# Kernel tuning notes

Hardware: AMD Instinct MI355X
Metric: run time of the kernel (lower is better)

The kernel has to match this reference:

```python
import jax, jax.numpy as jnp
import numpy as np

C_S, C_Z, S = 384, 128, 1024
D = 32
H = C_S // D
INF = 1e9
EPS = 1e-5


def rmsnorm(x, w, eps=EPS):
    ms = jnp.mean(jnp.square(x), axis=-1, keepdims=True)
    return x * jax.lax.rsqrt(ms + eps) * w


def setup_inputs() -> dict:
    key = jax.random.key(0)
    ks = jax.random.split(key, 12)
    inv_s = 1.0 / np.sqrt(C_S)
    inv_z = 1.0 / np.sqrt(C_Z)
    return {
        "s": jax.random.normal(ks[0], (S, C_S), jnp.float32),
        "z": jax.random.normal(ks[1], (S, S, C_Z), jnp.float32),
        "z_mask": jax.random.randint(ks[2], (S, S), 0, 2, jnp.int32),
        "w_s": jnp.ones((C_S,), jnp.float32),
        "w_z": jnp.ones((C_Z,), jnp.float32),
        "Wz": jax.random.normal(ks[3], (C_Z, H), jnp.float32) * inv_z,
        "Wq": jax.random.normal(ks[4], (C_S, H * D), jnp.float32) * inv_s,
        "Wk": jax.random.normal(ks[5], (C_S, H * D), jnp.float32) * inv_s,
        "Wv": jax.random.normal(ks[6], (C_S, H * D), jnp.float32) * inv_s,
        "Wg": jax.random.normal(ks[7], (C_S, C_S), jnp.float32) * inv_s,
        "bg": jnp.zeros((C_S,), jnp.float32),
        "Wo": jax.random.normal(ks[8], (C_S, C_S), jnp.float32) * inv_s,
        "bo": jnp.zeros((C_S,), jnp.float32),
    }


def reference(s, z, z_mask, w_s, w_z, Wz, Wq, Wk, Wv, Wg, bg, Wo, bo):
    s_n = rmsnorm(s, w_s)                      # [S, c_s]
    z_n = rmsnorm(z, w_z)                      # [S, S, c_z]
    q = (s_n @ Wq).reshape(S, H, D).transpose(1, 0, 2)  # [H, S, D]
    k = (s_n @ Wk).reshape(S, H, D).transpose(1, 0, 2)
    v = (s_n @ Wv).reshape(S, H, D).transpose(1, 0, 2)
    g = s_n @ Wg + bg                          # [S, c_s] (no sigmoid in source)
    # pair bias [H, S, S] + additive mask
    bias = jnp.einsum('ijc,ch->hij', z_n, Wz)
    bias = bias + jnp.where(z_mask != 0, 0.0, -INF)[None]
    scores = jnp.einsum('hid,hjd->hij', q, k) * (1.0 / np.sqrt(D)) + bias
    attn = jax.nn.softmax(scores, axis=-1)
    out = jnp.einsum('hij,hjd->hid', attn, v)  # [H, S, D]
    o = out.transpose(1, 0, 2).reshape(S, H * D)
    return ((o @ Wo + bo) * g).astype(jnp.float32)
```

## Files before the change

kernel.cpp:

```cpp
#include <hip/hip_runtime.h>
#include <hip/hip_fp16.h>

#define SQ 1024

typedef __attribute__((ext_vector_type(8))) short short8;
typedef __attribute__((ext_vector_type(4))) float f32x4;
typedef __attribute__((ext_vector_type(4))) int i32x4;
typedef __attribute__((ext_vector_type(2))) unsigned int u32x2;

#define MFMA16(a,b,c) __builtin_amdgcn_mfma_f32_16x16x32_bf16((a),(b),(c),0,0,0)

static __device__ __forceinline__ float bf2f(unsigned short u){
  union { unsigned int i; float f; } v; v.i = ((unsigned int)u) << 16; return v.f;
}
static __device__ __forceinline__ unsigned short f2bf(float f){
  union { float fv; unsigned int i; } v; v.fv = f;
  unsigned int r = v.i + 0x7fffu + ((v.i >> 16) & 1u);
  return (unsigned short)(r >> 16);
}
static __device__ __forceinline__ void split_store(float val, unsigned short* hi, unsigned short* lo, int idx){
  unsigned short h = f2bf(val);
  hi[idx] = h;
  lo[idx] = f2bf(val - bf2f(h));
}

static __device__ __forceinline__ void pack8(f32x4 u0, f32x4 u0b, short8& AHv, short8& ALv){
  unsigned int x0 = __float_as_uint(u0.x),  x1 = __float_as_uint(u0.y);
  unsigned int x2 = __float_as_uint(u0.z),  x3 = __float_as_uint(u0.w);
  unsigned int y0 = __float_as_uint(u0b.x), y1 = __float_as_uint(u0b.y);
  unsigned int y2 = __float_as_uint(u0b.z), y3 = __float_as_uint(u0b.w);
  float r0 = u0.x  - __uint_as_float(x0 & 0xffff0000u);
  float r1 = u0.y  - __uint_as_float(x1 & 0xffff0000u);
  float r2 = u0.z  - __uint_as_float(x2 & 0xffff0000u);
  float r3 = u0.w  - __uint_as_float(x3 & 0xffff0000u);
  float s0 = u0b.x - __uint_as_float(y0 & 0xffff0000u);
  float s1 = u0b.y - __uint_as_float(y1 & 0xffff0000u);
  float s2 = u0b.z - __uint_as_float(y2 & 0xffff0000u);
  float s3 = u0b.w - __uint_as_float(y3 & 0xffff0000u);
  union { unsigned int d[4]; short8 v; } AH, AL;
  AH.d[0] = (x0 >> 16) | (x1 & 0xffff0000u);
  AH.d[1] = (x2 >> 16) | (x3 & 0xffff0000u);
  AH.d[2] = (y0 >> 16) | (y1 & 0xffff0000u);
  AH.d[3] = (y2 >> 16) | (y3 & 0xffff0000u);
  AL.d[0] = (__float_as_uint(r0) >> 16) | (__float_as_uint(r1) & 0xffff0000u);
  AL.d[1] = (__float_as_uint(r2) >> 16) | (__float_as_uint(r3) & 0xffff0000u);
  AL.d[2] = (__float_as_uint(s0) >> 16) | (__float_as_uint(s1) & 0xffff0000u);
  AL.d[3] = (__float_as_uint(s2) >> 16) | (__float_as_uint(s3) & 0xffff0000u);
  AHv = AH.v; ALv = AL.v;
}

#define COMP4(v,e) ((e)==0?(v).x:(e)==1?(v).y:(e)==2?(v).z:(v).w)

#define QK_SCALE 0.17677669529663687f
#define MASK_NEG -60000.0f

__global__ __launch_bounds__(256) void prep_all(
    const float* __restrict__ Wq, const float* __restrict__ Wk,
    const float* __restrict__ Wv, const float* __restrict__ Wg,
    const float* __restrict__ Wo,
    const float* __restrict__ wz, const float* __restrict__ Wz,
    const float* __restrict__ s, const float* __restrict__ w_s,
    unsigned short* __restrict__ wt_hi, unsigned short* __restrict__ wt_lo,
    unsigned short* __restrict__ wwh, unsigned short* __restrict__ wwl2,
    unsigned short* __restrict__ s_hi, unsigned short* __restrict__ s_lo){
  __shared__ __align__(16) float tile[32][33];
  int bid = blockIdx.x;
  int t = threadIdx.x;
  if (bid < 720){
    int bx = bid % 60, by = bid / 60;
    int tx = t & 31, ty = t >> 5;
    int nt = bx * 32, kt = by * 32;
    int nb = nt / 384;
    const float* W = (nb==0)?Wq:(nb==1)?Wk:(nb==2)?Wv:(nb==3)?Wg:Wo;
    int nn0 = nt - nb*384;
    #pragma unroll
    for (int yy=0; yy<4; yy++){
      int k = kt + ty + yy*8;
      tile[ty + yy*8][tx] = W[k*384 + nn0 + tx];
    }
    __syncthreads();
    #pragma unroll
    for (int yy=0; yy<4; yy++){
      int n = nt + ty + yy*8;
      int k = kt + tx;
      float v = tile[tx][ty + yy*8];
      split_store(v, wt_hi, wt_lo, n*384 + k);
    }
  } else if (bid == 720){
    for (int idx = t; idx < 2048; idx += 256){
      int c = idx >> 4, h = idx & 15;
      float val = (h < 12) ? wz[c]*Wz[c*12 + h] : 0.f;
      unsigned short hh = f2bf(val);
      wwh[idx] = hh;
      wwl2[idx] = f2bf(val - bf2f(hh));
    }
  } else {
    int wv = t >> 6, lane = t & 63;
    int row = (bid - 721)*4 + wv;
    const float* sr = s + row*384;
    float v[6]; float ss = 0.f;
    #pragma unroll
    for (int q=0;q<6;q++){ v[q] = sr[lane + q*64]; ss += v[q]*v[q]; }
    #pragma unroll
    for (int m=1;m<64;m<<=1) ss += __shfl_xor(ss, m);
    float rs = rsqrtf(ss*(1.f/384.f) + 1e-5f);
    #pragma unroll
    for (int q=0;q<6;q++){
      int c = lane + q*64;
      split_store(v[q]*rs*w_s[c], s_hi, s_lo, row*384 + c);
    }
  }
}

__global__ __launch_bounds__(256,3) void qkvg_bias_k(
    const unsigned short* __restrict__ Ah, const unsigned short* __restrict__ Al,
    const unsigned short* __restrict__ Bh2, const unsigned short* __restrict__ Bl2,
    const float* __restrict__ bg,
    unsigned short* __restrict__ q_hi, unsigned short* __restrict__ q_lo,
    unsigned short* __restrict__ k_hi, unsigned short* __restrict__ k_lo,
    unsigned short* __restrict__ v_hi, unsigned short* __restrict__ v_lo,
    float* __restrict__ g,
    const float* __restrict__ z, const int* __restrict__ zm,
    const unsigned short* __restrict__ wwh, const unsigned short* __restrict__ wwl2,
    __half* __restrict__ biasH){
  __shared__ __align__(16) unsigned short lah[64*40], lal[64*40], lbh[64*40], lbl[64*40];
  __shared__ __align__(16) float rsbuf[4*16];
  int bid = blockIdx.x;
  int t = threadIdx.x, w = t >> 6, lane = t & 63;
  int fr = lane & 15, fg = lane >> 4;

  if (bid < 384){
    int m0 = (bid / 24) * 64, n0 = (bid % 24) * 64;
    f32x4 z4 = {0.f,0.f,0.f,0.f};
    f32x4 acc[4] = {z4, z4, z4, z4};
    int sr = t >> 2, sc = (t & 3) << 3;
    for (int k0 = 0; k0 < 384; k0 += 32){
      *(short8*)&lah[sr*40 + sc] = *(const short8*)&Ah[(m0+sr)*384 + k0 + sc];
      *(short8*)&lal[sr*40 + sc] = *(const short8*)&Al[(m0+sr)*384 + k0 + sc];
      *(short8*)&lbh[sr*40 + sc] = *(const short8*)&Bh2[(n0+sr)*384 + k0 + sc];
      *(short8*)&lbl[sr*40 + sc] = *(const short8*)&Bl2[(n0+sr)*384 + k0 + sc];
      __syncthreads();
      short8 a_h = *(short8*)&lah[(w*16+fr)*40 + (fg<<3)];
      short8 a_l = *(short8*)&lal[(w*16+fr)*40 + (fg<<3)];
      #pragma unroll
      for (int cf=0; cf<4; cf++){
        short8 b_h = *(short8*)&lbh[(cf*16+fr)*40 + (fg<<3)];
        short8 b_l = *(short8*)&lbl[(cf*16+fr)*40 + (fg<<3)];
        acc[cf] = MFMA16(a_h, b_h, acc[cf]);
        acc[cf] = MFMA16(a_h, b_l, acc[cf]);
        acc[cf] = MFMA16(a_l, b_h, acc[cf]);
      }
      __syncthreads();
    }
    int sec = n0 / 384;
    int nb0 = n0 - sec*384;
    #pragma unroll
    for (int cf=0; cf<4; cf++){
      #pragma unroll
      for (int jj=0; jj<4; jj++){
        int row = m0 + w*16 + (fg<<2) + jj;
        int nn = nb0 + cf*16 + fr;
        float val = acc[cf][jj];
        int hh = nn >> 5, dd = nn & 31;
        if (sec == 0)      split_store(val*QK_SCALE, q_hi, q_lo, (hh<<15) + (row<<5) + dd);
        else if (sec == 1) split_store(val, k_hi, k_lo, (hh<<15) + (row<<5) + dd);
        else if (sec == 2) split_store(val, v_hi, v_lo, (hh<<15) + dd*SQ + row);
        else               g[row*384 + nn] = val + bg[nn];
      }
    }
    return;
  }

  int wid = ((bid - 384) << 2) + w;

  short8 Bh[4], Bl[4];
  #pragma unroll
  for (int kt=0; kt<4; kt++){
    #pragma unroll
    for (int e=0; e<8; e++){
      int c = kt*32 + (fg<<3) + e;
      Bh[kt][e] = (short)wwh[(c<<4) + fr];
      Bl[kt][e] = (short)wwl2[(c<<4) + fr];
    }
  }

  f32x4 cA[8], cB[8];
  i32x4 zmA, zmB;

  #define LOADS(DST, ZMD, ST)                                             \
    {                                                                     \
      size_t tile = (size_t)(ST)*8192 + (size_t)wid;                      \
      const float* p = z + tile*2048 + fr*128 + (fg<<3);                  \
      DST[0] = __builtin_nontemporal_load((const f32x4*)(p));             \
      DST[1] = __builtin_nontemporal_load((const f32x4*)(p+4));           \
      DST[2] = __builtin_nontemporal_load((const f32x4*)(p+32));          \
      DST[3] = __builtin_nontemporal_load((const f32x4*)(p+36));          \
      DST[4] = __builtin_nontemporal_load((const f32x4*)(p+64));          \
      DST[5] = __builtin_nontemporal_load((const f32x4*)(p+68));          \
      DST[6] = __builtin_nontemporal_load((const f32x4*)(p+96));          \
      DST[7] = __builtin_nontemporal_load((const f32x4*)(p+100));         \
      int ii = (int)(tile >> 6), jj0 = ((int)tile & 63) << 4;             \
      ZMD = *(const i32x4*)&zm[ii*SQ + jj0 + (fg<<2)];                    \
    }

  #define COMPUTE(SRC, ZMD, ST)                                              \
    {                                                                        \
      f32x4 acc0 = {0.f,0.f,0.f,0.f};                                        \
      float ssq0 = 0.f;                                                      \
      _Pragma("unroll")                                                      \
      for (int kt=0; kt<4; kt++){                                            \
        f32x4 u0  = SRC[kt*2];                                               \
        f32x4 u0b = SRC[kt*2+1];                                             \
        ssq0 = fmaf(u0.x,u0.x,ssq0);   ssq0 = fmaf(u0.y,u0.y,ssq0);          \
        ssq0 = fmaf(u0.z,u0.z,ssq0);   ssq0 = fmaf(u0.w,u0.w,ssq0);          \
        ssq0 = fmaf(u0b.x,u0b.x,ssq0); ssq0 = fmaf(u0b.y,u0b.y,ssq0);        \
        ssq0 = fmaf(u0b.z,u0b.z,ssq0); ssq0 = fmaf(u0b.w,u0b.w,ssq0);        \
        short8 AHv, ALv;                                                     \
        pack8(u0, u0b, AHv, ALv);                                            \
        acc0 = MFMA16(AHv, Bh[kt], acc0);                                    \
        acc0 = MFMA16(AHv, Bl[kt], acc0);                                    \
        acc0 = MFMA16(ALv, Bh[kt], acc0);                                    \
      }                                                                      \
      ssq0 += __shfl_xor(ssq0, 16); ssq0 += __shfl_xor(ssq0, 32);            \
      if (lane < 16)                                                         \
        rsbuf[w*16 + lane] = rsqrtf(ssq0*(1.0f/128.0f) + 1e-5f);             \
      int jo = fg << 2;                                                      \
      f32x4 rs0 = *(const f32x4*)&rsbuf[w*16 + jo];                          \
      f32x4 mk0;                                                             \
      mk0.x = (ZMD.x != 0) ? 0.f : MASK_NEG;                                 \
      mk0.y = (ZMD.y != 0) ? 0.f : MASK_NEG;                                 \
      mk0.z = (ZMD.z != 0) ? 0.f : MASK_NEG;                                 \
      mk0.w = (ZMD.w != 0) ? 0.f : MASK_NEG;                                 \
      if (fr < 12){                                                          \
        size_t tile = (size_t)(ST)*8192 + (size_t)wid;                       \
        int ii = (int)(tile >> 6), jj0 = ((int)tile & 63) << 4;              \
        size_t hb = (size_t)ii*12288 + (size_t)fr*SQ + jj0;                  \
        union { __half2 h2[2]; u32x2 u; } pk;                                \
        pk.h2[0] = __floats2half2_rn(fmaf(acc0[0], rs0.x, mk0.x),            \
                                     fmaf(acc0[1], rs0.y, mk0.y));           \
        pk.h2[1] = __floats2half2_rn(fmaf(acc0[2], rs0.z, mk0.z),            \
                                     fmaf(acc0[3], rs0.w, mk0.w));           \
        __builtin_nontemporal_store(pk.u, (u32x2*)&biasH[hb + jo]);          \
      }                                                                      \
    }

  LOADS(cA, zmA, 0)
  #pragma unroll 1
  for (int st = 0; st < 8; st += 2){
    LOADS(cB, zmB, st+1)
    __builtin_amdgcn_sched_barrier(0);
    COMPUTE(cA, zmA, st)
    if (st+2 < 8) LOADS(cA, zmA, st+2)
    __builtin_amdgcn_sched_barrier(0);
    COMPUTE(cB, zmB, st+1)
  }
  #undef LOADS
  #undef COMPUTE
}

__global__ __launch_bounds__(256) void attn_k(
    const unsigned short* __restrict__ qh_, const unsigned short* __restrict__ ql_,
    const unsigned short* __restrict__ kh_, const unsigned short* __restrict__ kl_,
    const unsigned short* __restrict__ vh_, const unsigned short* __restrict__ vl_,
    const __half* __restrict__ biasH,
    unsigned short* __restrict__ oh_, unsigned short* __restrict__ ol_){
  __shared__ __align__(16) float Sl[16*1028];
  __shared__ __align__(16) float Opart[4*512];
  __shared__ float rsl[16];
  int t = threadIdx.x, wv = t >> 6, lane = t & 63;
  int fr = lane & 15, fg = lane >> 4;

  #pragma unroll 1
  for (int u = 0; u < 2; u++){
    int unit = (blockIdx.x << 1) | u;
    int h = unit >> 6;
    int i0 = (unit & 63) << 4;
    int hbase = h << 15;
    const unsigned short* qh = qh_ + hbase; const unsigned short* ql = ql_ + hbase;
    const unsigned short* kh = kh_ + hbase; const unsigned short* kl = kl_ + hbase;
    const unsigned short* vh = vh_ + hbase; const unsigned short* vl = vl_ + hbase;

    short8 aqh = *(const short8*)&qh[((i0 + fr) << 5) + (fg << 3)];
    short8 aql = *(const short8*)&ql[((i0 + fr) << 5) + (fg << 3)];

    #pragma unroll 4
    for (int jt = 0; jt < 16; jt++){
      int j0 = (wv << 8) + (jt << 4);
      short8 bkh = *(const short8*)&kh[((j0 + fr) << 5) + (fg << 3)];
      short8 bkl = *(const short8*)&kl[((j0 + fr) << 5) + (fg << 3)];
      f32x4 a = {0.f,0.f,0.f,0.f};
      a = MFMA16(aqh, bkh, a);
      a = MFMA16(aqh, bkl, a);
      a = MFMA16(aql, bkh, a);
      #pragma unroll
      for (int jj=0; jj<4; jj++)
        Sl[(fg*4 + jj)*1028 + j0 + fr] = a[jj];
    }
    __syncthreads();

    {
      int row = t >> 4, l16 = t & 15;
      float* Srow = &Sl[row*1028];
      const __half* brow = biasH + (size_t)(i0 + row)*12288 + (size_t)h*SQ;
      float mx = -3.0e38f;
      #pragma unroll 4
      for (int cc=0; cc<16; cc++){
        int j = (l16 + cc*16) << 2;
        f32x4 sv = *(f32x4*)&Srow[j];
        union { u32x2 uu; __half2 h2[2]; } bv;
        bv.uu = *(const u32x2*)&brow[j];
        float2 f01 = __half22float2(bv.h2[0]);
        float2 f23 = __half22float2(bv.h2[1]);
        sv.x += f01.x; sv.y += f01.y; sv.z += f23.x; sv.w += f23.y;
        *(f32x4*)&Srow[j] = sv;
        mx = fmaxf(mx, fmaxf(fmaxf(sv.x, sv.y), fmaxf(sv.z, sv.w)));
      }
      mx = fmaxf(mx, __shfl_xor(mx, 1));
      mx = fmaxf(mx, __shfl_xor(mx, 2));
      mx = fmaxf(mx, __shfl_xor(mx, 4));
      mx = fmaxf(mx, __shfl_xor(mx, 8));
      float sm = 0.f;
      #pragma unroll 4
      for (int cc=0; cc<16; cc++){
        int j = (l16 + cc*16) << 2;
        f32x4 sv = *(f32x4*)&Srow[j];
        sv.x = __expf(sv.x - mx); sv.y = __expf(sv.y - mx);
        sv.z = __expf(sv.z - mx); sv.w = __expf(sv.w - mx);
        *(f32x4*)&Srow[j] = sv;
        sm += sv.x + sv.y + sv.z + sv.w;
      }
      sm += __shfl_xor(sm, 1);
      sm += __shfl_xor(sm, 2);
      sm += __shfl_xor(sm, 4);
      sm += __shfl_xor(sm, 8);
      if (l16 == 0) rsl[row] = 1.0f / sm;
    }
    __syncthreads();

    f32x4 o0 = {0.f,0.f,0.f,0.f}, o1 = {0.f,0.f,0.f,0.f};
    #pragma unroll 2
    for (int kk=0; kk<8; kk++){
      int k0 = (wv << 8) + (kk << 5);
      f32x4 pa = *(const f32x4*)&Sl[fr*1028 + k0 + (fg<<3)];
      f32x4 pb = *(const f32x4*)&Sl[fr*1028 + k0 + (fg<<3) + 4];
      short8 ph, pl;
      pack8(pa, pb, ph, pl);
      short8 v0h = *(const short8*)&vh[fr*SQ + k0 + (fg<<3)];
      short8 v0l = *(const short8*)&vl[fr*SQ + k0 + (fg<<3)];
      short8 v1h = *(const short8*)&vh[(16+fr)*SQ + k0 + (fg<<3)];
      short8 v1l = *(const short8*)&vl[(16+fr)*SQ + k0 + (fg<<3)];
      o0 = MFMA16(ph, v0h, o0); o0 = MFMA16(ph, v0l, o0); o0 = MFMA16(pl, v0h, o0);
      o1 = MFMA16(ph, v1h, o1); o1 = MFMA16(ph, v1l, o1); o1 = MFMA16(pl, v1h, o1);
    }
    {
      float* op = &Opart[wv*512];
      #pragma unroll
      for (int jj=0; jj<4; jj++){
        op[(fg*4 + jj)*32 + fr]      = o0[jj];
        op[(fg*4 + jj)*32 + 16 + fr] = o1[jj];
      }
    }
    __syncthreads();

    #pragma unroll
    for (int uu=0; uu<2; uu++){
      int idx = t + uu*256;
      int q = idx >> 5, d = idx & 31;
      float v = Opart[q*32 + d] + Opart[512 + q*32 + d]
              + Opart[1024 + q*32 + d] + Opart[1536 + q*32 + d];
      v *= rsl[q];
      split_store(v, oh_, ol_, (i0 + q)*384 + (h << 5) + d);
    }
    __syncthreads();
  }
}

__global__ __launch_bounds__(256) void gemm_out_k(
    const unsigned short* __restrict__ Ah, const unsigned short* __restrict__ Al,
    const unsigned short* __restrict__ Bh, const unsigned short* __restrict__ Bl,
    const float* __restrict__ bo, const float* __restrict__ g,
    float* __restrict__ out){
  __shared__ __align__(16) unsigned short lah[32*40], lal[32*40], lbh[64*40], lbl[64*40];
  int t = threadIdx.x, wv = t >> 6, lane = t & 63;
  int m0 = blockIdx.y * 32, n0 = blockIdx.x * 64;
  int fr = lane & 15, fg = lane >> 4;
  int ms = (wv & 1) << 4, ns = (wv >> 1) << 5;
  f32x4 z4 = {0.f,0.f,0.f,0.f};
  f32x4 acc[2] = {z4, z4};
  int sr = t >> 2, sc = (t & 3) << 3;
  for (int k0 = 0; k0 < 384; k0 += 32){
    if (t < 128){
      *(short8*)&lah[sr*40 + sc] = *(const short8*)&Ah[(m0+sr)*384 + k0 + sc];
      *(short8*)&lal[sr*40 + sc] = *(const short8*)&Al[(m0+sr)*384 + k0 + sc];
    }
    *(short8*)&lbh[sr*40 + sc] = *(const short8*)&Bh[(n0+sr)*384 + k0 + sc];
    *(short8*)&lbl[sr*40 + sc] = *(const short8*)&Bl[(n0+sr)*384 + k0 + sc];
    __syncthreads();
    short8 a_h = *(short8*)&lah[(ms+fr)*40 + (fg<<3)];
    short8 a_l = *(short8*)&lal[(ms+fr)*40 + (fg<<3)];
    #pragma unroll
    for (int cf=0; cf<2; cf++){
      short8 b_h = *(short8*)&lbh[(ns + cf*16 + fr)*40 + (fg<<3)];
      short8 b_l = *(short8*)&lbl[(ns + cf*16 + fr)*40 + (fg<<3)];
      acc[cf] = MFMA16(a_h, b_h, acc[cf]);
      acc[cf] = MFMA16(a_h, b_l, acc[cf]);
      acc[cf] = MFMA16(a_l, b_h, acc[cf]);
    }
    __syncthreads();
  }
  #pragma unroll
  for (int cf=0; cf<2; cf++){
    #pragma unroll
    for (int jj=0; jj<4; jj++){
      int row = m0 + ms + (fg<<2) + jj;
      int col = n0 + ns + cf*16 + fr;
      out[row*384 + col] = (acc[cf][jj] + bo[col]) * g[row*384 + col];
    }
  }
}

extern "C" void kernel_launch(void* const* d_in, const int* in_sizes, int n_in,
                              void* d_out, int out_size, void* d_ws, size_t ws_size,
                              hipStream_t stream) {
  const float* s   = (const float*)d_in[0];
  const float* z   = (const float*)d_in[1];
  const int*   zm  = (const int*)d_in[2];
  const float* w_s = (const float*)d_in[3];
  const float* w_z = (const float*)d_in[4];
  const float* Wz  = (const float*)d_in[5];
  const float* Wq  = (const float*)d_in[6];
  const float* Wk  = (const float*)d_in[7];
  const float* Wv  = (const float*)d_in[8];
  const float* Wg  = (const float*)d_in[9];
  const float* bg  = (const float*)d_in[10];
  const float* Wo  = (const float*)d_in[11];
  const float* bo  = (const float*)d_in[12];
  float* out = (float*)d_out;
  char* ws = (char*)d_ws;

  unsigned short* s_hi  = (unsigned short*)(ws + 0);
  unsigned short* s_lo  = (unsigned short*)(ws + 786432);
  unsigned short* wt_hi = (unsigned short*)(ws + 1572864);
  unsigned short* wt_lo = (unsigned short*)(ws + 3047424);
  unsigned short* wwh   = (unsigned short*)(ws + 4521984);
  unsigned short* wwl2  = (unsigned short*)(ws + 4526080);
  unsigned short* q_hi  = (unsigned short*)(ws + 4532224);
  unsigned short* q_lo  = (unsigned short*)(ws + 5318656);
  unsigned short* k_hi  = (unsigned short*)(ws + 6105088);
  unsigned short* k_lo  = (unsigned short*)(ws + 6891520);
  unsigned short* v_hi  = (unsigned short*)(ws + 7677952);
  unsigned short* v_lo  = (unsigned short*)(ws + 8464384);
  float*          gbuf  = (float*)(ws + 9250816);
  unsigned short* o_hi  = (unsigned short*)(ws + 10823680);
  unsigned short* o_lo  = (unsigned short*)(ws + 11610112);
  __half*         biasH = (__half*)(ws + 12396544);

  prep_all<<<977, 256, 0, stream>>>(Wq, Wk, Wv, Wg, Wo, w_z, Wz, s, w_s,
                                    wt_hi, wt_lo, wwh, wwl2, s_hi, s_lo);
  qkvg_bias_k<<<2432, 256, 0, stream>>>(s_hi, s_lo, wt_hi, wt_lo, bg,
                                        q_hi, q_lo, k_hi, k_lo, v_hi, v_lo, gbuf,
                                        z, zm, wwh, wwl2, biasH);
  attn_k<<<384, 256, 0, stream>>>(q_hi, q_lo, k_hi, k_lo, v_hi, v_lo, biasH, o_hi, o_lo);
  gemm_out_k<<<dim3(6,32), 256, 0, stream>>>(o_hi, o_lo,
                                             wt_hi + 1536*384, wt_lo + 1536*384,
                                             bo, gbuf, out);
}
```

Before: 204.6 us.

## Stream z tiles through LDS with async global_load_lds multi-stage pipeline

Replaces the register double-buffered z loads in the pair-bias path with direct global-to-LDS async loads (global_load_lds), staged four half-tiles deep per wave with manual vmcnt waits and an XOR swizzle to avoid bank conflicts. Mask values are prefetched up front for all eight tiles. The aim is to keep more memory requests in flight and free registers while streaming the large z tensor. In exchange it uses about 64KB of LDS per block and lowers the launch-bounds occupancy hint from 3 to 2 blocks, which may reduce latency hiding, and the GEMM branch now shares the same large LDS allocation.

```diff
diff --git a/kernel.cpp b/kernel.cpp
--- a/kernel.cpp
+++ b/kernel.cpp
@@ -22,6 +22,15 @@
   unsigned short h = f2bf(val);
   hi[idx] = h;
   lo[idx] = f2bf(val - bf2f(h));
+}
+
+static __device__ __forceinline__ void gld_lds16(const float* g, float* d){
+  __builtin_amdgcn_global_load_lds(
+    static_cast<const unsigned int __attribute__((address_space(1)))*>(
+        (const void __attribute__((address_space(1)))*)g),
+    static_cast<unsigned int __attribute__((address_space(3)))*>(
+        (void __attribute__((address_space(3)))*)d),
+    16, 0, 0);
 }
 
 static __device__ __forceinline__ void pack8(f32x4 u0, f32x4 u0b, short8& AHv, short8& ALv){
@@ -112,7 +121,7 @@
   }
 }
 
-__global__ __launch_bounds__(256,3) void qkvg_bias_k(
+__global__ __launch_bounds__(256,2) void qkvg_bias_k(
     const unsigned short* __restrict__ Ah, const unsigned short* __restrict__ Al,
     const unsigned short* __restrict__ Bh2, const unsigned short* __restrict__ Bl2,
     const float* __restrict__ bg,
@@ -123,13 +132,16 @@
     const float* __restrict__ z, const int* __restrict__ zm,
     const unsigned short* __restrict__ wwh, const unsigned short* __restrict__ wwl2,
     __half* __restrict__ biasH){
-  __shared__ __align__(16) unsigned short lah[64*40], lal[64*40], lbh[64*40], lbl[64*40];
-  __shared__ __align__(16) float rsbuf[4*16];
+  __shared__ __align__(16) char smem[65792];
   int bid = blockIdx.x;
   int t = threadIdx.x, w = t >> 6, lane = t & 63;
   int fr = lane & 15, fg = lane >> 4;
 
   if (bid < 384){
+    unsigned short* lah = (unsigned short*)smem;
+    unsigned short* lal = (unsigned short*)(smem + 5120);
+    unsigned short* lbh = (unsigned short*)(smem + 10240);
+    unsigned short* lbl = (unsigned short*)(smem + 15360);
     int m0 = (bid / 24) * 64, n0 = (bid % 24) * 64;
     f32x4 z4 = {0.f,0.f,0.f,0.f};
     f32x4 acc[4] = {z4, z4, z4, z4};
@@ -172,6 +184,9 @@
   }
 
   int wid = ((bid - 384) << 2) + w;
+  float* zbuf  = (float*)smem;
+  float* rsbuf = (float*)(smem + 65536);
+  int q4 = lane >> 4, l16 = lane & 15;
 
   short8 Bh[4], Bl[4];
   #pragma unroll
@@ -184,78 +199,88 @@
     }
   }
 
-  f32x4 cA[8], cB[8];
-  i32x4 zmA, zmB;
-
-  #define LOADS(DST, ZMD, ST)                                             \
-    {                                                                     \
-      size_t tile = (size_t)(ST)*8192 + (size_t)wid;                      \
-      const float* p = z + tile*2048 + fr*128 + (fg<<3);                  \
-      DST[0] = __builtin_nontemporal_load((const f32x4*)(p));             \
-      DST[1] = __builtin_nontemporal_load((const f32x4*)(p+4));           \
-      DST[2] = __builtin_nontemporal_load((const f32x4*)(p+32));          \
-      DST[3] = __builtin_nontemporal_load((const f32x4*)(p+36));          \
-      DST[4] = __builtin_nontemporal_load((const f32x4*)(p+64));          \
-      DST[5] = __builtin_nontemporal_load((const f32x4*)(p+68));          \
-      DST[6] = __builtin_nontemporal_load((const f32x4*)(p+96));          \
-      DST[7] = __builtin_nontemporal_load((const f32x4*)(p+100));         \
-      int ii = (int)(tile >> 6), jj0 = ((int)tile & 63) << 4;             \
-      ZMD = *(const i32x4*)&zm[ii*SQ + jj0 + (fg<<2)];                    \
-    }
-
-  #define COMPUTE(SRC, ZMD, ST)                                              \
+  i32x4 zmv[8];
+  #pragma unroll
+  for (int tt=0; tt<8; tt++){
+    size_t tile = (size_t)tt*8192 + (size_t)wid;
+    int ii = (int)(tile >> 6), jj0 = ((int)tile & 63) << 4;
+    zmv[tt] = *(const i32x4*)&zm[ii*SQ + jj0 + (fg<<2)];
+  }
+
+  #define STAGE(HT)                                                          \
     {                                                                        \
-      f32x4 acc0 = {0.f,0.f,0.f,0.f};                                        \
-      float ssq0 = 0.f;                                                      \
+      size_t tile = (size_t)((HT)>>1)*8192 + (size_t)wid;                    \
+      const float* zs = z + tile*2048 + (((HT)&1)<<6);                       \
+      float* db = zbuf + ((w<<2) + ((HT)&3))*1024;                           \
       _Pragma("unroll")                                                      \
-      for (int kt=0; kt<4; kt++){                                            \
-        f32x4 u0  = SRC[kt*2];                                               \
-        f32x4 u0b = SRC[kt*2+1];                                             \
-        ssq0 = fmaf(u0.x,u0.x,ssq0);   ssq0 = fmaf(u0.y,u0.y,ssq0);          \
-        ssq0 = fmaf(u0.z,u0.z,ssq0);   ssq0 = fmaf(u0.w,u0.w,ssq0);          \
-        ssq0 = fmaf(u0b.x,u0b.x,ssq0); ssq0 = fmaf(u0b.y,u0b.y,ssq0);        \
-        ssq0 = fmaf(u0b.z,u0b.z,ssq0); ssq0 = fmaf(u0b.w,u0b.w,ssq0);        \
-        short8 AHv, ALv;                                                     \
-        pack8(u0, u0b, AHv, ALv);                                            \
-        acc0 = MFMA16(AHv, Bh[kt], acc0);                                    \
-        acc0 = MFMA16(AHv, Bl[kt], acc0);                                    \
-        acc0 = MFMA16(ALv, Bh[kt], acc0);                                    \
+      for (int n=0; n<4; ++n){                                               \
+        int r = (n<<2) + q4;                                                 \
+        gld_lds16(zs + r*128 + ((l16 ^ (r&7)) << 2), db + n*256);            \
       }                                                                      \
-      ssq0 += __shfl_xor(ssq0, 16); ssq0 += __shfl_xor(ssq0, 32);            \
-      if (lane < 16)                                                         \
-        rsbuf[w*16 + lane] = rsqrtf(ssq0*(1.0f/128.0f) + 1e-5f);             \
-      int jo = fg << 2;                                                      \
-      f32x4 rs0 = *(const f32x4*)&rsbuf[w*16 + jo];                          \
-      f32x4 mk0;                                                             \
-      mk0.x = (ZMD.x != 0) ? 0.f : MASK_NEG;                                 \
-      mk0.y = (ZMD.y != 0) ? 0.f : MASK_NEG;                                 \
-      mk0.z = (ZMD.z != 0) ? 0.f : MASK_NEG;                                 \
-      mk0.w = (ZMD.w != 0) ? 0.f : MASK_NEG;                                 \
-      if (fr < 12){                                                          \
-        size_t tile = (size_t)(ST)*8192 + (size_t)wid;                       \
-        int ii = (int)(tile >> 6), jj0 = ((int)tile & 63) << 4;              \
-        size_t hb = (size_t)ii*12288 + (size_t)fr*SQ + jj0;                  \
-        union { __half2 h2[2]; u32x2 u; } pk;                                \
-        pk.h2[0] = __floats2half2_rn(fmaf(acc0[0], rs0.x, mk0.x),            \
-                                     fmaf(acc0[1], rs0.y, mk0.y));           \
-        pk.h2[1] = __floats2half2_rn(fmaf(acc0[2], rs0.z, mk0.z),            \
-                                     fmaf(acc0[3], rs0.w, mk0.w));           \
-        __builtin_nontemporal_store(pk.u, (u32x2*)&biasH[hb + jo]);          \
-      }                                                                      \
-    }
-
-  LOADS(cA, zmA, 0)
-  #pragma unroll 1
-  for (int st = 0; st < 8; st += 2){
-    LOADS(cB, zmB, st+1)
-    __builtin_amdgcn_sched_barrier(0);
-    COMPUTE(cA, zmA, st)
-    if (st+2 < 8) LOADS(cA, zmA, st+2)
-    __builtin_amdgcn_sched_barrier(0);
-    COMPUTE(cB, zmB, st+1)
-  }
-  #undef LOADS
-  #undef COMPUTE
+    }
+
+  STAGE(0) STAGE(1) STAGE(2)
+
+  f32x4 acc0 = {0.f,0.f,0.f,0.f};
+  float ssq0 = 0.f;
+  int r7 = fr & 7;
+
+  #pragma unroll
+  for (int ht = 0; ht < 16; ++ht){
+    if (ht + 3 < 16) STAGE(ht+3)
+    if (ht < 13)       asm volatile("s_waitcnt vmcnt(12)" ::: "memory");
+    else if (ht == 13) asm volatile("s_waitcnt vmcnt(8)"  ::: "memory");
+    else if (ht == 14) asm volatile("s_waitcnt vmcnt(4)"  ::: "memory");
+    else               asm volatile("s_waitcnt vmcnt(0)"  ::: "memory");
+
+    if ((ht & 1) == 0){ acc0.x=0.f; acc0.y=0.f; acc0.z=0.f; acc0.w=0.f; ssq0 = 0.f; }
+
+    const int zb = ((w<<2) + (ht&3))*1024;
+    #pragma unroll
+    for (int ktl=0; ktl<2; ++ktl){
+      int kt = ((ht&1)<<1) + ktl;
+      int g0 = (ktl<<3) + (fg<<1);
+      f32x4 u0  = *(const f32x4*)&zbuf[zb + (fr<<6) + ((g0 ^ r7) << 2)];
+      f32x4 u0b = *(const f32x4*)&zbuf[zb + (fr<<6) + (((g0+1) ^ r7) << 2)];
+      ssq0 = fmaf(u0.x,u0.x,ssq0);   ssq0 = fmaf(u0.y,u0.y,ssq0);
+      ssq0 = fmaf(u0.z,u0.z,ssq0);   ssq0 = fmaf(u0.w,u0.w,ssq0);
+      ssq0 = fmaf(u0b.x,u0b.x,ssq0); ssq0 = fmaf(u0b.y,u0b.y,ssq0);
+      ssq0 = fmaf(u0b.z,u0b.z,ssq0); ssq0 = fmaf(u0b.w,u0b.w,ssq0);
+      short8 AHv, ALv;
+      pack8(u0, u0b, AHv, ALv);
+      acc0 = MFMA16(AHv, Bh[kt], acc0);
+      acc0 = MFMA16(AHv, Bl[kt], acc0);
+      acc0 = MFMA16(ALv, Bh[kt], acc0);
+    }
+
+    if (ht & 1){
+      int tt = ht >> 1;
+      float sq = ssq0;
+      sq += __shfl_xor(sq, 16); sq += __shfl_xor(sq, 32);
+      if (lane < 16)
+        rsbuf[(w<<4) + lane] = rsqrtf(sq*(1.0f/128.0f) + 1e-5f);
+      int jo = fg << 2;
+      f32x4 rs0 = *(const f32x4*)&rsbuf[(w<<4) + jo];
+      i32x4 Z = zmv[tt];
+      f32x4 mk0;
+      mk0.x = (Z.x != 0) ? 0.f : MASK_NEG;
+      mk0.y = (Z.y != 0) ? 0.f : MASK_NEG;
+      mk0.z = (Z.z != 0) ? 0.f : MASK_NEG;
+      mk0.w = (Z.w != 0) ? 0.f : MASK_NEG;
+      if (fr < 12){
+        size_t tile = (size_t)tt*8192 + (size_t)wid;
+        int ii = (int)(tile >> 6), jj0 = ((int)tile & 63) << 4;
+        size_t hb = (size_t)ii*12288 + (size_t)fr*SQ + jj0;
+        union { __half2 h2[2]; u32x2 u; } pk;
+        pk.h2[0] = __floats2half2_rn(fmaf(acc0[0], rs0.x, mk0.x),
+                                     fmaf(acc0[1], rs0.y, mk0.y));
+        pk.h2[1] = __floats2half2_rn(fmaf(acc0[2], rs0.z, mk0.z),
+                                     fmaf(acc0[3], rs0.w, mk0.w));
+        __builtin_nontemporal_store(pk.u, (u32x2*)&biasH[hb + jo]);
+      }
+    }
+  }
+  #undef STAGE
 }
 
 __global__ __launch_bounds__(256) void attn_k(
```

Measured after the change: 187.2 us. -8.5%, faster.
